# Optimization experiments

Measured on AMD Instinct MI355X. Metric: run time of the kernel, lower is better.

Reference implementation:

```python
import jax, jax.numpy as jnp
import numpy as np

N_NODES = 50000


def gcn_conv(x, W, b, src, dst, ew, n_nodes):
    """PyG GCNConv: out = D^{-1/2}(A + I)D^{-1/2} (x @ W) + b, A weighted by ew.

    Self loops (weight 1) are handled analytically instead of appending edges.
    """
    h = x @ W  # [N, out]
    # degree includes self-loop weight of 1
    deg = jax.ops.segment_sum(ew, dst, num_segments=n_nodes) + 1.0  # [N]
    dinv = jnp.where(deg > 0, jax.lax.rsqrt(deg), 0.0)
    norm = dinv[src] * ew * dinv[dst]  # [E]
    # message = norm * h[src], scatter-add to dst
    agg = jax.ops.segment_sum(h[src] * norm[:, None], dst, num_segments=n_nodes)
    # self-loop contribution: dinv[i] * 1 * dinv[i] * h[i]
    agg = agg + h * (dinv * dinv)[:, None]
    return agg + b


def setup_inputs() -> dict:
    key = jax.random.key(0)
    k = jax.random.split(key, 8)
    n, e, d_in, d_h = N_NODES, 600000, 128, 128
    x = jax.random.normal(k[0], (n, d_in), dtype=jnp.float32)
    edge_index = jax.random.randint(k[1], (2, e), 0, n, dtype=jnp.int64)
    edge_attr = jax.random.uniform(k[2], (e,), dtype=jnp.float32)
    s1 = 1.0 / np.sqrt(d_in)
    s2 = 1.0 / np.sqrt(d_h)
    W1 = jax.random.uniform(k[3], (d_in, d_h), jnp.float32, -s1, s1)
    b1 = jnp.zeros((d_h,), jnp.float32)
    W2 = jax.random.uniform(k[4], (d_h, d_h), jnp.float32, -s2, s2)
    b2 = jnp.zeros((d_h,), jnp.float32)
    return {"x": x, "edge_index": edge_index, "edge_attr": edge_attr,
            "W1": W1, "b1": b1, "W2": W2, "b2": b2}


def reference(x, edge_index, edge_attr, W1, b1, W2, b2):
    src, dst = edge_index[0], edge_index[1]
    h = gcn_conv(x, W1, b1, src, dst, edge_attr, N_NODES)
    h = jax.nn.relu(h)
    # dropout is identity in eval mode (deterministic reference)
    out = gcn_conv(h, W2, b2, src, dst, edge_attr, N_NODES)
    return out
```

## Files before the change

### kernel.cpp

```cpp
#include <hip/hip_runtime.h>
#include <stdint.h>

#define D 128

typedef __bf16 bf16x8 __attribute__((ext_vector_type(8)));
typedef float f32x4 __attribute__((ext_vector_type(4)));

__device__ inline float bf2f(unsigned short u) {
    return __uint_as_float((unsigned)u << 16);
}
__device__ inline unsigned short f2bf(float f) {
    unsigned u = __float_as_uint(f);
    return (unsigned short)((u + 0x7FFF + ((u >> 16) & 1)) >> 16);
}

__global__ __launch_bounds__(256) void k_prep(const float* __restrict__ W1,
                                              unsigned short* __restrict__ Wt1,
                                              const float* __restrict__ W2,
                                              unsigned short* __restrict__ Wt2,
                                              unsigned long long* __restrict__ pk, int n) {
    __shared__ float t[128 * 132];
    const int tid = threadIdx.x;
    if (blockIdx.x < 2) {
        const float* W = (blockIdx.x == 0) ? W1 : W2;
        unsigned short* Wt = (blockIdx.x == 0) ? Wt1 : Wt2;
        for (int i = tid; i < 128 * 32; i += 256) {
            int r = i >> 5, c = i & 31;
            float4 v = *(const float4*)(W + r * 128 + c * 4);
            float* dp = &t[r * 132 + c * 4];
            dp[0] = v.x; dp[1] = v.y; dp[2] = v.z; dp[3] = v.w;
        }
        __syncthreads();
        for (int i = tid; i < 128 * 32; i += 256) {
            int nn = i >> 5, c = i & 31;
            ushort4 o;
            o.x = f2bf(t[(c * 4 + 0) * 132 + nn]);
            o.y = f2bf(t[(c * 4 + 1) * 132 + nn]);
            o.z = f2bf(t[(c * 4 + 2) * 132 + nn]);
            o.w = f2bf(t[(c * 4 + 3) * 132 + nn]);
            *(ushort4*)(Wt + nn * 128 + c * 4) = o;
        }
    } else {
        int i = (blockIdx.x - 2) * 256 + tid;
        if (i < n) pk[i] = 0ULL;
    }
}

template <bool IN_BF16>
__device__ inline void mfma_body(unsigned short* sW, unsigned short* sX,
                                 const void* __restrict__ Xv,
                                 const unsigned short* __restrict__ Wt,
                                 unsigned short* __restrict__ H, int n, int blk) {
    const int tid = threadIdx.x;
    const int row0 = blk * 64;

    for (int i = tid; i < 128 * 16; i += 256) {
        int r = i >> 4, c = i & 15;
        *(int4*)(&sW[r * 136 + c * 8]) = *(const int4*)(Wt + r * 128 + c * 8);
    }
    if (IN_BF16) {
        const unsigned short* Xh = (const unsigned short*)Xv;
        for (int i = tid; i < 64 * 16; i += 256) {
            int r = i >> 4, c = i & 15;
            int gr = row0 + r;
            int4 v = make_int4(0, 0, 0, 0);
            if (gr < n) v = *(const int4*)(Xh + (size_t)gr * 128 + c * 8);
            *(int4*)(&sX[r * 136 + c * 8]) = v;
        }
    } else {
        const float* Xf = (const float*)Xv;
        for (int i = tid; i < 64 * 32; i += 256) {
            int r = i >> 5, c = i & 31;
            int gr = row0 + r;
            float4 v = make_float4(0.f, 0.f, 0.f, 0.f);
            if (gr < n) v = *(const float4*)(Xf + (size_t)gr * 128 + c * 4);
            ushort4 o;
            o.x = f2bf(v.x); o.y = f2bf(v.y); o.z = f2bf(v.z); o.w = f2bf(v.w);
            *(ushort4*)(&sX[r * 136 + c * 4]) = o;
        }
    }
    __syncthreads();

    const int lane = tid & 63;
    const int wv = tid >> 6;
    const int qm = lane & 15;
    const int quad = lane >> 4;

    f32x4 acc[8];
#pragma unroll
    for (int i = 0; i < 8; ++i) acc[i] = (f32x4){0.f, 0.f, 0.f, 0.f};

#pragma unroll
    for (int kb = 0; kb < 4; ++kb) {
        const int koff = kb * 32 + quad * 8;
        bf16x8 a = *(const bf16x8*)(&sX[(wv * 16 + qm) * 136 + koff]);
#pragma unroll
        for (int n0 = 0; n0 < 8; ++n0) {
            bf16x8 b = *(const bf16x8*)(&sW[(n0 * 16 + qm) * 136 + koff]);
            acc[n0] = __builtin_amdgcn_mfma_f32_16x16x32_bf16(a, b, acc[n0], 0, 0, 0);
        }
    }

    __syncthreads();
    unsigned short* sE = sX;
#pragma unroll
    for (int n0 = 0; n0 < 8; ++n0)
#pragma unroll
        for (int r = 0; r < 4; ++r)
            sE[(wv * 16 + quad * 4 + r) * 136 + n0 * 16 + qm] = f2bf(acc[n0][r]);
    __syncthreads();

    const int row_in = lane >> 2;
    const int c0 = (lane & 3) * 4;
    const int grow = row0 + wv * 16 + row_in;
    if (grow < n) {
#pragma unroll
        for (int j = 0; j < 4; ++j)
            *(int4*)(H + (size_t)grow * 128 + (c0 + j) * 8) =
                *(const int4*)(&sE[(wv * 16 + row_in) * 136 + (c0 + j) * 8]);
    }
}

__global__ __launch_bounds__(256) void k_cm(const float* __restrict__ X,
                                            const unsigned short* __restrict__ Wt,
                                            unsigned short* __restrict__ H, int n, int gb,
                                            const int* __restrict__ ei,
                                            const float* __restrict__ ew,
                                            unsigned long long* __restrict__ pk,
                                            int* __restrict__ rank, int E) {
    __shared__ unsigned short sW[128 * 136];
    __shared__ unsigned short sX[64 * 136];
    if (blockIdx.x < gb) {
        mfma_body<false>(sW, sX, (const void*)X, Wt, H, n, blockIdx.x);
    } else {
        int e = (blockIdx.x - gb) * 256 + threadIdx.x;
        if (e < E) {
            int d = ei[E + e];
            unsigned int fx = (unsigned int)(ew[e] * 16777216.0f);
            unsigned long long old =
                atomicAdd(&pk[d], (1ULL << 32) | (unsigned long long)fx);
            rank[e] = (int)(old >> 32);
        }
    }
}

__global__ __launch_bounds__(256) void k_mfma2(const unsigned short* __restrict__ X,
                                               const unsigned short* __restrict__ Wt,
                                               unsigned short* __restrict__ H, int n) {
    __shared__ unsigned short sW[128 * 136];
    __shared__ unsigned short sX[64 * 136];
    mfma_body<true>(sW, sX, (const void*)X, Wt, H, n, blockIdx.x);
}

__global__ __launch_bounds__(256) void k_scanA(const unsigned long long* __restrict__ pk,
                                               int* rowstart, int* bsums, int n) {
    __shared__ int tmp[256];
    int tid = threadIdx.x;
    int i = blockIdx.x * 256 + tid;
    int v = (i < n) ? (int)(pk[i] >> 32) : 0;
    tmp[tid] = v;
    __syncthreads();
    for (int off = 1; off < 256; off <<= 1) {
        int t = (tid >= off) ? tmp[tid - off] : 0;
        __syncthreads();
        tmp[tid] += t;
        __syncthreads();
    }
    if (i < n) rowstart[i] = tmp[tid] - v;
    if (tid == 255) bsums[blockIdx.x] = tmp[255];
}

__global__ __launch_bounds__(256) void k_scanBC(int* rowstart, const int* __restrict__ bsums,
                                                const unsigned long long* __restrict__ pk,
                                                int* cnt, float* dinv, int n) {
    __shared__ int sred[4];
    int tid = threadIdx.x;
    int v = (tid < (int)blockIdx.x) ? bsums[tid] : 0;
#pragma unroll
    for (int off = 32; off; off >>= 1) v += __shfl_down(v, off);
    if ((tid & 63) == 0) sred[tid >> 6] = v;
    __syncthreads();
    int total = sred[0] + sred[1] + sred[2] + sred[3];
    int i = blockIdx.x * 256 + tid;
    if (i < n) {
        rowstart[i] += total;
        unsigned long long pv = pk[i];
        cnt[i] = (int)(pv >> 32);
        float deg = 1.0f + (float)(unsigned int)(pv & 0xFFFFFFFFu) * (1.0f / 16777216.0f);
        dinv[i] = rsqrtf(deg);
    }
}

__global__ __launch_bounds__(256) void k_edges(const int* __restrict__ ei,
                                               const float* __restrict__ ew,
                                               const float* __restrict__ dinv,
                                               const int* __restrict__ rowstart,
                                               const int* __restrict__ rank,
                                               int2* __restrict__ erec, int E) {
    int e = blockIdx.x * 256 + threadIdx.x;
    if (e < E) {
        int s = ei[e];
        int d = ei[E + e];
        int p = rowstart[d] + rank[e];
        float nm = dinv[s] * ew[e] * dinv[d];
        erec[p] = make_int2(s, __float_as_int(nm));
    }
}

template <bool OUT_BF16>
__global__ __launch_bounds__(256) void k_gather(const ushort4* __restrict__ H4,
                                                const int2* __restrict__ erec,
                                                const int* __restrict__ rowstart,
                                                const int* __restrict__ cnt,
                                                const float* __restrict__ dinv,
                                                const float4* __restrict__ bias4,
                                                void* __restrict__ OUTv, int n) {
    const int lane = threadIdx.x & 31;
    const int node = blockIdx.x * 8 + (threadIdx.x >> 5);
    if (node >= n) return;
    const int start = rowstart[node];
    const int m = cnt[node];
    const float di = dinv[node];
    const float dii = di * di;

    float4 b = bias4[lane];
    ushort4 h = H4[(size_t)node * 32 + lane];
    float ax = b.x + dii * bf2f(h.x);
    float ay = b.y + dii * bf2f(h.y);
    float az = b.z + dii * bf2f(h.z);
    float aw = b.w + dii * bf2f(h.w);

    int j = 0;
    for (; j + 4 <= m; j += 4) {
        const int base = start + j;
        int2 e0 = erec[base + 0], e1 = erec[base + 1];
        int2 e2 = erec[base + 2], e3 = erec[base + 3];
        float w0 = __int_as_float(e0.y), w1 = __int_as_float(e1.y);
        float w2 = __int_as_float(e2.y), w3 = __int_as_float(e3.y);
        ushort4 v0 = H4[(size_t)e0.x * 32 + lane];
        ushort4 v1 = H4[(size_t)e1.x * 32 + lane];
        ushort4 v2 = H4[(size_t)e2.x * 32 + lane];
        ushort4 v3 = H4[(size_t)e3.x * 32 + lane];
        ax += w0 * bf2f(v0.x); ay += w0 * bf2f(v0.y); az += w0 * bf2f(v0.z); aw += w0 * bf2f(v0.w);
        ax += w1 * bf2f(v1.x); ay += w1 * bf2f(v1.y); az += w1 * bf2f(v1.z); aw += w1 * bf2f(v1.w);
        ax += w2 * bf2f(v2.x); ay += w2 * bf2f(v2.y); az += w2 * bf2f(v2.z); aw += w2 * bf2f(v2.w);
        ax += w3 * bf2f(v3.x); ay += w3 * bf2f(v3.y); az += w3 * bf2f(v3.z); aw += w3 * bf2f(v3.w);
    }
    for (; j < m; ++j) {
        int2 er = erec[start + j];
        float w = __int_as_float(er.y);
        ushort4 v = H4[(size_t)er.x * 32 + lane];
        ax += w * bf2f(v.x); ay += w * bf2f(v.y); az += w * bf2f(v.z); aw += w * bf2f(v.w);
    }
    if (OUT_BF16) {
        ushort4 o;
        o.x = f2bf(fmaxf(ax, 0.f)); o.y = f2bf(fmaxf(ay, 0.f));
        o.z = f2bf(fmaxf(az, 0.f)); o.w = f2bf(fmaxf(aw, 0.f));
        ((ushort4*)OUTv)[(size_t)node * 32 + lane] = o;
    } else {
        float4 o; o.x = ax; o.y = ay; o.z = az; o.w = aw;
        ((float4*)OUTv)[(size_t)node * 32 + lane] = o;
    }
}

extern "C" void kernel_launch(void* const* d_in, const int* in_sizes, int n_in,
                              void* d_out, int out_size, void* d_ws, size_t ws_size,
                              hipStream_t stream) {
    const float* x  = (const float*)d_in[0];
    const int*   ei = (const int*)d_in[1];
    const float* ew = (const float*)d_in[2];
    const float* W1 = (const float*)d_in[3];
    const float* b1 = (const float*)d_in[4];
    const float* W2 = (const float*)d_in[5];
    const float* b2 = (const float*)d_in[6];
    float* out = (float*)d_out;

    const int N = in_sizes[0] / D;
    const int E = in_sizes[2];

    char* p = (char*)d_ws;
    auto alloc = [&](size_t bytes) {
        void* r = (void*)p;
        p += (bytes + 255) & ~(size_t)255;
        return r;
    };
    unsigned long long* pk = (unsigned long long*)alloc((size_t)N * 8);
    float* dinv     = (float*)alloc((size_t)N * 4);
    int*   cnt      = (int*)alloc((size_t)N * 4);
    int*   rowstart = (int*)alloc((size_t)N * 4);
    int*   bsums    = (int*)alloc(1024 * 4);
    int*   rank     = (int*)alloc((size_t)E * 4);
    int2*  erec     = (int2*)alloc((size_t)E * 8);
    unsigned short* B1  = (unsigned short*)alloc((size_t)N * D * 2);
    unsigned short* B2h = (unsigned short*)alloc((size_t)N * D * 2);
    unsigned short* Wt1 = (unsigned short*)alloc(128 * 128 * 2);
    unsigned short* Wt2 = (unsigned short*)alloc(128 * 128 * 2);

    const int nb = (N + 255) / 256;
    const int eb = (E + 255) / 256;
    const int gb = (N + 63) / 64;
    const int hb = (N + 7) / 8;

    k_prep<<<2 + nb, 256, 0, stream>>>(W1, Wt1, W2, Wt2, pk, N);
    k_cm<<<gb + eb, 256, 0, stream>>>(x, Wt1, B1, N, gb, ei, ew, pk, rank, E);
    k_scanA<<<nb, 256, 0, stream>>>(pk, rowstart, bsums, N);
    k_scanBC<<<nb, 256, 0, stream>>>(rowstart, bsums, pk, cnt, dinv, N);
    k_edges<<<eb, 256, 0, stream>>>(ei, ew, dinv, rowstart, rank, erec, E);
    k_gather<true><<<hb, 256, 0, stream>>>((const ushort4*)B1, erec, rowstart, cnt,
                                           dinv, (const float4*)b1, (void*)B2h, N);
    k_mfma2<<<gb, 256, 0, stream>>>(B2h, Wt2, B1, N);
    k_gather<false><<<hb, 256, 0, stream>>>((const ushort4*)B1, erec, rowstart, cnt,
                                            dinv, (const float4*)b2, (void*)out, N);
}
```

Baseline: 221.4 us.

## Load MFMA operands directly from global memory and batch edge work per thread

The dense matmul body stops staging W and X tiles in shared memory. A and B fragments are now read straight from global memory (W from L2), and shared memory is kept only for the output transpose. This cuts LDS use so more blocks fit per CU (launch bounds set to 4) and removes a barrier. The edge-count and edge-scatter kernels now handle 4 and 2 edges per thread so loads are issued ahead of the atomics. The cost is that every wave re-reads W from global/L2 instead of sharing one LDS copy.

```diff
diff --git a/kernel.cpp b/kernel.cpp
--- a/kernel.cpp
+++ b/kernel.cpp
@@ -47,45 +47,20 @@
 }
 
 template <bool IN_BF16>
-__device__ inline void mfma_body(unsigned short* sW, unsigned short* sX,
+__device__ inline void mfma_body(unsigned short* sE,
                                  const void* __restrict__ Xv,
                                  const unsigned short* __restrict__ Wt,
                                  unsigned short* __restrict__ H, int n, int blk) {
     const int tid = threadIdx.x;
     const int row0 = blk * 64;
-
-    for (int i = tid; i < 128 * 16; i += 256) {
-        int r = i >> 4, c = i & 15;
-        *(int4*)(&sW[r * 136 + c * 8]) = *(const int4*)(Wt + r * 128 + c * 8);
-    }
-    if (IN_BF16) {
-        const unsigned short* Xh = (const unsigned short*)Xv;
-        for (int i = tid; i < 64 * 16; i += 256) {
-            int r = i >> 4, c = i & 15;
-            int gr = row0 + r;
-            int4 v = make_int4(0, 0, 0, 0);
-            if (gr < n) v = *(const int4*)(Xh + (size_t)gr * 128 + c * 8);
-            *(int4*)(&sX[r * 136 + c * 8]) = v;
-        }
-    } else {
-        const float* Xf = (const float*)Xv;
-        for (int i = tid; i < 64 * 32; i += 256) {
-            int r = i >> 5, c = i & 31;
-            int gr = row0 + r;
-            float4 v = make_float4(0.f, 0.f, 0.f, 0.f);
-            if (gr < n) v = *(const float4*)(Xf + (size_t)gr * 128 + c * 4);
-            ushort4 o;
-            o.x = f2bf(v.x); o.y = f2bf(v.y); o.z = f2bf(v.z); o.w = f2bf(v.w);
-            *(ushort4*)(&sX[r * 136 + c * 4]) = o;
-        }
-    }
-    __syncthreads();
-
     const int lane = tid & 63;
     const int wv = tid >> 6;
     const int qm = lane & 15;
     const int quad = lane >> 4;
 
+    const int arow = row0 + wv * 16 + qm;
+    const int ar = (arow < n) ? arow : (n - 1);
+
     f32x4 acc[8];
 #pragma unroll
     for (int i = 0; i < 8; ++i) acc[i] = (f32x4){0.f, 0.f, 0.f, 0.f};
@@ -93,16 +68,27 @@
 #pragma unroll
     for (int kb = 0; kb < 4; ++kb) {
         const int koff = kb * 32 + quad * 8;
-        bf16x8 a = *(const bf16x8*)(&sX[(wv * 16 + qm) * 136 + koff]);
+        bf16x8 a;
+        if (IN_BF16) {
+            a = *(const bf16x8*)((const unsigned short*)Xv + (size_t)ar * 128 + koff);
+        } else {
+            const float* Xf = (const float*)Xv + (size_t)ar * 128 + koff;
+            float4 v0 = *(const float4*)(Xf);
+            float4 v1 = *(const float4*)(Xf + 4);
+            union { bf16x8 v; ushort4 u[2]; } cv;
+            cv.u[0].x = f2bf(v0.x); cv.u[0].y = f2bf(v0.y);
+            cv.u[0].z = f2bf(v0.z); cv.u[0].w = f2bf(v0.w);
+            cv.u[1].x = f2bf(v1.x); cv.u[1].y = f2bf(v1.y);
+            cv.u[1].z = f2bf(v1.z); cv.u[1].w = f2bf(v1.w);
+            a = cv.v;
+        }
 #pragma unroll
         for (int n0 = 0; n0 < 8; ++n0) {
-            bf16x8 b = *(const bf16x8*)(&sW[(n0 * 16 + qm) * 136 + koff]);
+            bf16x8 b = *(const bf16x8*)(Wt + (n0 * 16 + qm) * 128 + koff);
             acc[n0] = __builtin_amdgcn_mfma_f32_16x16x32_bf16(a, b, acc[n0], 0, 0, 0);
         }
     }
 
-    __syncthreads();
-    unsigned short* sE = sX;
 #pragma unroll
     for (int n0 = 0; n0 < 8; ++n0)
 #pragma unroll
@@ -121,35 +107,44 @@
     }
 }
 
-__global__ __launch_bounds__(256) void k_cm(const float* __restrict__ X,
-                                            const unsigned short* __restrict__ Wt,
-                                            unsigned short* __restrict__ H, int n, int gb,
-                                            const int* __restrict__ ei,
-                                            const float* __restrict__ ew,
-                                            unsigned long long* __restrict__ pk,
-                                            int* __restrict__ rank, int E) {
-    __shared__ unsigned short sW[128 * 136];
-    __shared__ unsigned short sX[64 * 136];
+__global__ __launch_bounds__(256, 4) void k_cm(const float* __restrict__ X,
+                                               const unsigned short* __restrict__ Wt,
+                                               unsigned short* __restrict__ H, int n, int gb,
+                                               const int* __restrict__ ei,
+                                               const float* __restrict__ ew,
+                                               unsigned long long* __restrict__ pk,
+                                               int* __restrict__ rank, int E) {
+    __shared__ unsigned short sE[64 * 136];
     if (blockIdx.x < gb) {
-        mfma_body<false>(sW, sX, (const void*)X, Wt, H, n, blockIdx.x);
+        mfma_body<false>(sE, (const void*)X, Wt, H, n, blockIdx.x);
     } else {
-        int e = (blockIdx.x - gb) * 256 + threadIdx.x;
-        if (e < E) {
-            int d = ei[E + e];
-            unsigned int fx = (unsigned int)(ew[e] * 16777216.0f);
-            unsigned long long old =
-                atomicAdd(&pk[d], (1ULL << 32) | (unsigned long long)fx);
-            rank[e] = (int)(old >> 32);
-        }
-    }
-}
-
-__global__ __launch_bounds__(256) void k_mfma2(const unsigned short* __restrict__ X,
-                                               const unsigned short* __restrict__ Wt,
-                                               unsigned short* __restrict__ H, int n) {
-    __shared__ unsigned short sW[128 * 136];
-    __shared__ unsigned short sX[64 * 136];
-    mfma_body<true>(sW, sX, (const void*)X, Wt, H, n, blockIdx.x);
+        const int base = (blockIdx.x - gb) * 1024 + threadIdx.x;
+        int d[4]; float w[4];
+        bool ok[4];
+#pragma unroll
+        for (int k = 0; k < 4; ++k) {
+            int e = base + k * 256;
+            ok[k] = (e < E);
+            d[k] = ok[k] ? ei[E + e] : 0;
+            w[k] = ok[k] ? ew[e] : 0.f;
+        }
+#pragma unroll
+        for (int k = 0; k < 4; ++k) {
+            if (ok[k]) {
+                unsigned int fx = (unsigned int)(w[k] * 16777216.0f);
+                unsigned long long old =
+                    atomicAdd(&pk[d[k]], (1ULL << 32) | (unsigned long long)fx);
+                rank[base + k * 256] = (int)(old >> 32);
+            }
+        }
+    }
+}
+
+__global__ __launch_bounds__(256, 4) void k_mfma2(const unsigned short* __restrict__ X,
+                                                  const unsigned short* __restrict__ Wt,
+                                                  unsigned short* __restrict__ H, int n) {
+    __shared__ unsigned short sE[64 * 136];
+    mfma_body<true>(sE, (const void*)X, Wt, H, n, blockIdx.x);
 }
 
 __global__ __launch_bounds__(256) void k_scanA(const unsigned long long* __restrict__ pk,
@@ -197,13 +192,17 @@
                                                const int* __restrict__ rowstart,
                                                const int* __restrict__ rank,
                                                int2* __restrict__ erec, int E) {
-    int e = blockIdx.x * 256 + threadIdx.x;
-    if (e < E) {
-        int s = ei[e];
-        int d = ei[E + e];
-        int p = rowstart[d] + rank[e];
-        float nm = dinv[s] * ew[e] * dinv[d];
-        erec[p] = make_int2(s, __float_as_int(nm));
+    const int base = blockIdx.x * 512 + threadIdx.x;
+#pragma unroll
+    for (int k = 0; k < 2; ++k) {
+        int e = base + k * 256;
+        if (e < E) {
+            int s = ei[e];
+            int d = ei[E + e];
+            int p = rowstart[d] + rank[e];
+            float nm = dinv[s] * ew[e] * dinv[d];
+            erec[p] = make_int2(s, __float_as_int(nm));
+        }
     }
 }
 
@@ -296,16 +295,17 @@
     unsigned short* Wt1 = (unsigned short*)alloc(128 * 128 * 2);
     unsigned short* Wt2 = (unsigned short*)alloc(128 * 128 * 2);
 
-    const int nb = (N + 255) / 256;
-    const int eb = (E + 255) / 256;
-    const int gb = (N + 63) / 64;
-    const int hb = (N + 7) / 8;
+    const int nb  = (N + 255) / 256;
+    const int eb2 = (E + 511) / 512;
+    const int eb4 = (E + 1023) / 1024;
+    const int gb  = (N + 63) / 64;
+    const int hb  = (N + 7) / 8;
 
     k_prep<<<2 + nb, 256, 0, stream>>>(W1, Wt1, W2, Wt2, pk, N);
-    k_cm<<<gb + eb, 256, 0, stream>>>(x, Wt1, B1, N, gb, ei, ew, pk, rank, E);
+    k_cm<<<gb + eb4, 256, 0, stream>>>(x, Wt1, B1, N, gb, ei, ew, pk, rank, E);
     k_scanA<<<nb, 256, 0, stream>>>(pk, rowstart, bsums, N);
     k_scanBC<<<nb, 256, 0, stream>>>(rowstart, bsums, pk, cnt, dinv, N);
-    k_edges<<<eb, 256, 0, stream>>>(ei, ew, dinv, rowstart, rank, erec, E);
+    k_edges<<<eb2, 256, 0, stream>>>(ei, ew, dinv, rowstart, rank, erec, E);
     k_gather<true><<<hb, 256, 0, stream>>>((const ushort4*)B1, erec, rowstart, cnt,
                                            dinv, (const float4*)b1, (void*)B2h, N);
     k_mfma2<<<gb, 256, 0, stream>>>(B2h, Wt2, B1, N);
```

Result: slower. 231.1 us (+4.4%).
